# Kernel tuning notes

Hardware: AMD Instinct MI355X
Metric: run time of the kernel (lower is better)

The kernel has to match this reference:

```python
import jax, jax.numpy as jnp
import numpy as np

N_HEADS = 16
KQ_DIM = 64
EMB_DIM = 1024
CTX_DIM = 1024
EPS = 1e-5

def _layernorm(x, w, b):
    # LayerNorm over last dim (kq_dim), elementwise affine
    mu = jnp.mean(x, axis=-1, keepdims=True)
    var = jnp.mean(jnp.square(x - mu), axis=-1, keepdims=True)
    return (x - mu) * jax.lax.rsqrt(var + EPS) * w + b

def setup_inputs() -> dict:
    key = jax.random.key(0)
    ks = jax.random.split(key, 10)
    B, SQ, SK = 2, 2048, 2048
    inner = N_HEADS * KQ_DIM
    s_e = 1.0 / np.sqrt(EMB_DIM)
    s_c = 1.0 / np.sqrt(CTX_DIM)
    s_i = 1.0 / np.sqrt(inner)
    return {
        "emb": jax.random.normal(ks[0], (B, SQ, EMB_DIM), jnp.float32),
        "context": jax.random.normal(ks[1], (B, SK, CTX_DIM), jnp.float32),
        "Wq": jax.random.uniform(ks[2], (inner, EMB_DIM), jnp.float32, -s_e, s_e),
        "Wk": jax.random.uniform(ks[3], (inner, CTX_DIM), jnp.float32, -s_c, s_c),
        "Wv": jax.random.uniform(ks[4], (inner, CTX_DIM), jnp.float32, -s_c, s_c),
        "Wu": jax.random.uniform(ks[5], (EMB_DIM, inner), jnp.float32, -s_i, s_i),
        "bu": jax.random.uniform(ks[6], (EMB_DIM,), jnp.float32, -s_i, s_i),
        "qn_w": jnp.ones((KQ_DIM,), jnp.float32),
        "qn_b": jnp.zeros((KQ_DIM,), jnp.float32),
        "kn_w": jnp.ones((KQ_DIM,), jnp.float32),
        "kn_b": jnp.zeros((KQ_DIM,), jnp.float32),
    }

def reference(emb, context, Wq, Wk, Wv, Wu, bu, qn_w, qn_b, kn_w, kn_b):
    B, SQ, _ = emb.shape
    SK = context.shape[1]
    # projections (no bias), reshape to [B, H, S, D]
    q = (emb @ Wq.T).reshape(B, SQ, N_HEADS, KQ_DIM).transpose(0, 2, 1, 3)
    k = (context @ Wk.T).reshape(B, SK, N_HEADS, KQ_DIM).transpose(0, 2, 1, 3)
    v = (context @ Wv.T).reshape(B, SK, N_HEADS, KQ_DIM).transpose(0, 2, 1, 3)
    q = _layernorm(q, qn_w, qn_b)
    k = _layernorm(k, kn_w, kn_b)
    scale = 1.0 / jnp.sqrt(jnp.asarray(KQ_DIM, emb.dtype))
    attn = jnp.einsum('bhqd,bhkd->bhqk', q, k) * scale
    attn = jax.nn.softmax(attn, axis=-1)
    out = jnp.einsum('bhqk,bhkd->bhqd', attn, v)
    out = out.transpose(0, 2, 1, 3).reshape(B, SQ, N_HEADS * KQ_DIM)
    return out @ Wu.T + bu
```

## Files before the change

### kernel.cpp

```cpp
#include <hip/hip_runtime.h>


typedef __attribute__((ext_vector_type(8)))  short bf16x8;
typedef __attribute__((ext_vector_type(4)))  short bf16x4;
typedef __attribute__((ext_vector_type(4)))  float f32x4;
typedef __attribute__((ext_vector_type(16))) float f32x16;
typedef __attribute__((ext_vector_type(4)))  unsigned int u32x4;

#define SM_SCALE 0.18033688f

typedef __attribute__((address_space(1))) const void cg_void;
typedef __attribute__((address_space(3))) void lds_void_t;

__device__ __forceinline__ void gl_lds16(const void* g, void* l){
  __builtin_amdgcn_global_load_lds((cg_void*)g, (lds_void_t*)l, 16, 0, 0);
}

__device__ __forceinline__ short f2b(float f){
  unsigned int u;
  __builtin_memcpy(&u, &f, 4);
  u += 0x7fffu + ((u >> 16) & 1u);
  return (short)(u >> 16);
}

__device__ __forceinline__ unsigned int cvtpk(float a, float b){
  unsigned int r;
  asm("v_cvt_pk_bf16_f32 %0, %1, %2" : "=v"(r) : "v"(a), "v"(b));
  return r;
}

__global__ __launch_bounds__(256) void cvt6_kernel(
    const float* __restrict__ emb, const float* __restrict__ ctx,
    const float* __restrict__ Wq, const float* __restrict__ Wk,
    const float* __restrict__ Wv, const float* __restrict__ Wu,
    short* __restrict__ o_emb, short* __restrict__ o_ctx,
    short* __restrict__ o_wq, short* __restrict__ o_wk,
    short* __restrict__ o_wv, short* __restrict__ o_wu)
{
  const long M1 = 1024L * 1024L, M4 = 4L * M1;
  long e = ((long)blockIdx.x * 256 + threadIdx.x) * 4;
  if (e >= 12L * M1) return;
  const float* src; short* dst; long off;
  if      (e <     M4)      { src = emb; dst = o_emb; off = e;           }
  else if (e < 2 * M4)      { src = ctx; dst = o_ctx; off = e - M4;      }
  else if (e < 2 * M4 + M1) { src = Wq;  dst = o_wq;  off = e - 2 * M4;  }
  else if (e < 2 * M4 + 2*M1){src = Wk;  dst = o_wk;  off = e - 2*M4 - M1;}
  else if (e < 2 * M4 + 3*M1){src = Wv;  dst = o_wv;  off = e - 2*M4 - 2*M1;}
  else                      { src = Wu;  dst = o_wu;  off = e - 2*M4 - 3*M1;}
  f32x4 v = *(const f32x4*)(src + off);
  bf16x4 o;
  o[0] = f2b(v[0]); o[1] = f2b(v[1]); o[2] = f2b(v[2]); o[3] = f2b(v[3]);
  *(bf16x4*)(dst + off) = o;
}

__global__ __launch_bounds__(256, 3) void gemm_qkv_kernel(
    const short* __restrict__ embh, const short* __restrict__ ctxh,
    const short* __restrict__ Wqh, const short* __restrict__ Wkh,
    const short* __restrict__ Wvh,
    short* __restrict__ qo, short* __restrict__ ko, short* __restrict__ vto,
    const float* __restrict__ qw, const float* __restrict__ qb,
    const float* __restrict__ kw, const float* __restrict__ kb)
{
  const int K = 1024;
  __shared__ short As[128 * 64];
  __shared__ short Bs[128 * 64];
  const int tid  = threadIdx.x;
  const int wave = tid >> 6, lane = tid & 63;
  const int quad = lane >> 4, r16 = lane & 15;
  const int wm = (wave >> 1) * 64, wn = (wave & 1) * 64;

  const int task = blockIdx.y;
  int bn, bm, N;
  const short *A, *B;
  if (task == 2){
    bn = (blockIdx.x & 31) * 128; bm = (blockIdx.x >> 5) * 128; N = 4096;
    A = Wvh; B = ctxh;
  } else {
    bm = (blockIdx.x & 31) * 128; bn = (blockIdx.x >> 5) * 128; N = 1024;
    A = task ? ctxh : embh; B = task ? Wkh : Wqh;
  }

  f32x4 acc[4][4];
#pragma unroll
  for (int i = 0; i < 4; i++)
#pragma unroll
    for (int j = 0; j < 4; j++)
      acc[i][j] = (f32x4){0.f, 0.f, 0.f, 0.f};

  const int sr7 = (lane >> 3) & 7;
  const size_t arow = (size_t)(bm + wave * 8 + (lane >> 3)) * K
                      + (((lane & 7) ^ sr7) * 8);
  const size_t brow = (size_t)(bn + wave * 8 + (lane >> 3)) * K
                      + (((lane & 7) ^ sr7) * 8);
  const int sw = ((quad ^ (r16 & 7)) << 3);

  for (int k0 = 0; k0 < K; k0 += 64){
#pragma unroll
    for (int i = 0; i < 4; i++)
      gl_lds16(A + arow + (size_t)32 * i * K + k0, &As[wave * 512 + i * 2048]);
#pragma unroll
    for (int i = 0; i < 4; i++)
      gl_lds16(B + brow + (size_t)32 * i * K + k0, &Bs[wave * 512 + i * 2048]);
    __syncthreads();
#pragma unroll
    for (int kk = 0; kk < 2; kk++){
      const int off = sw ^ (kk << 5);
      bf16x8 af[4], bq[4];
#pragma unroll
      for (int i = 0; i < 4; i++)
        af[i] = *(const bf16x8*)(&As[(wm + i*16 + r16) * 64 + off]);
#pragma unroll
      for (int j = 0; j < 4; j++)
        bq[j] = *(const bf16x8*)(&Bs[(wn + j*16 + r16) * 64 + off]);
#pragma unroll
      for (int i = 0; i < 4; i++)
#pragma unroll
        for (int j = 0; j < 4; j++)
          acc[i][j] = __builtin_amdgcn_mfma_f32_16x16x32_bf16(af[i], bq[j], acc[i][j], 0, 0, 0);
    }
    __syncthreads();
  }

  if (task < 2){
    short* Ch = task ? ko : qo;
    const float* lw = task ? kw : qw;
    const float* lb = task ? kb : qb;
    const float post = task ? 1.0f : SM_SCALE;
    float wv[4], bv[4];
#pragma unroll
    for (int j = 0; j < 4; j++){
      wv[j] = lw[j*16 + r16] * post;
      bv[j] = lb[j*16 + r16] * post;
    }
#pragma unroll
    for (int i = 0; i < 4; i++){
#pragma unroll
      for (int t = 0; t < 4; t++){
        float a[4];
#pragma unroll
        for (int j = 0; j < 4; j++) a[j] = acc[i][j][t];
        float s = a[0] + a[1] + a[2] + a[3];
        s += __shfl_xor(s, 1); s += __shfl_xor(s, 2);
        s += __shfl_xor(s, 4); s += __shfl_xor(s, 8);
        const float mu = s * 0.015625f;
        float d[4], sq = 0.f;
#pragma unroll
        for (int j = 0; j < 4; j++){ d[j] = a[j] - mu; sq += d[j]*d[j]; }
        sq += __shfl_xor(sq, 1); sq += __shfl_xor(sq, 2);
        sq += __shfl_xor(sq, 4); sq += __shfl_xor(sq, 8);
        const float si = rsqrtf(sq * 0.015625f + 1e-5f);
        const size_t row = (size_t)(bm + wm + i*16 + quad*4 + t);
#pragma unroll
        for (int j = 0; j < 4; j++)
          Ch[row * 1024 + (bn + wn + j*16 + r16)] = f2b(d[j] * si * wv[j] + bv[j]);
      }
    }
  } else {
#pragma unroll
    for (int i = 0; i < 4; i++){
#pragma unroll
      for (int j = 0; j < 4; j++){
        const int p = (r16 & 3) | ((j & 1) << 2) | (((r16 >> 2) & 1) << 3)
                      | (((r16 >> 3) & 1) << 4);
        const int col = ((bn + wn + j*16 + r16) & ~31) | p;
#pragma unroll
        for (int t = 0; t < 4; t++){
          const size_t row = (size_t)(bm + wm + i*16 + quad*4 + t);
          vto[row * (size_t)N + col] = f2b(acc[i][j][t]);
        }
      }
    }
  }
}

__global__ __launch_bounds__(256, 4) void gemm_out_kernel(
    const short* __restrict__ A, const short* __restrict__ B,
    float* __restrict__ Cf, const float* __restrict__ bias)
{
  const int K = 1024, N = 1024;
  __shared__ short As[64 * 64];
  __shared__ short Bs[64 * 64];
  const int tid  = threadIdx.x;
  const int wave = tid >> 6, lane = tid & 63;
  const int quad = lane >> 4, r16 = lane & 15;
  const int wm = (wave >> 1) * 32, wn = (wave & 1) * 32;
  const int bm = blockIdx.x * 64, bn = blockIdx.y * 64;

  f32x4 acc[2][2];
#pragma unroll
  for (int i = 0; i < 2; i++)
#pragma unroll
    for (int j = 0; j < 2; j++)
      acc[i][j] = (f32x4){0.f, 0.f, 0.f, 0.f};

  const int sr7 = (lane >> 3) & 7;
  const size_t arow = (size_t)(bm + wave * 8 + (lane >> 3)) * K
                      + (((lane & 7) ^ sr7) * 8);
  const size_t brow = (size_t)(bn + wave * 8 + (lane >> 3)) * K
                      + (((lane & 7) ^ sr7) * 8);
  const int sw = ((quad ^ (r16 & 7)) << 3);

  for (int k0 = 0; k0 < K; k0 += 64){
#pragma unroll
    for (int i = 0; i < 2; i++){
      gl_lds16(A + arow + (size_t)32 * i * K + k0, &As[wave * 512 + i * 2048]);
      gl_lds16(B + brow + (size_t)32 * i * K + k0, &Bs[wave * 512 + i * 2048]);
    }
    __syncthreads();
#pragma unroll
    for (int kk = 0; kk < 2; kk++){
      const int off = sw ^ (kk << 5);
      bf16x8 af[2], bq[2];
#pragma unroll
      for (int i = 0; i < 2; i++)
        af[i] = *(const bf16x8*)(&As[(wm + i*16 + r16) * 64 + off]);
#pragma unroll
      for (int j = 0; j < 2; j++)
        bq[j] = *(const bf16x8*)(&Bs[(wn + j*16 + r16) * 64 + off]);
#pragma unroll
      for (int i = 0; i < 2; i++)
#pragma unroll
        for (int j = 0; j < 2; j++)
          acc[i][j] = __builtin_amdgcn_mfma_f32_16x16x32_bf16(af[i], bq[j], acc[i][j], 0, 0, 0);
    }
    __syncthreads();
  }

#pragma unroll
  for (int i = 0; i < 2; i++){
#pragma unroll
    for (int j = 0; j < 2; j++){
      const int col = bn + wn + j*16 + r16;
#pragma unroll
      for (int t = 0; t < 4; t++){
        const size_t row = (size_t)(bm + wm + i*16 + quad*4 + t);
        Cf[row * N + col] = acc[i][j][t] + bias[col];
      }
    }
  }
}

__global__ __launch_bounds__(256, 2) void flash2_kernel(
    const short* __restrict__ Q, const short* __restrict__ K,
    const short* __restrict__ Vt, short* __restrict__ O)
{
  __shared__ __align__(16) long long smem8[8192];
  short* Ks  = (short*)smem8;
  short* Vts = Ks + 16384;
  float* scr = (float*)smem8;

  const int tid = threadIdx.x;
  const int wave = tid >> 6, lane = tid & 63;
  const int half = wave >> 1, wg = wave & 1;
  const int hh = lane >> 5, q5 = lane & 31;
  const int h = blockIdx.x, qb = blockIdx.y, b = blockIdx.z;
  const int q0 = qb * 128 + wg * 64;

  const size_t kbase = ((size_t)b * 2048) * 1024 + (size_t)h * 64;
  const size_t vbase = ((size_t)h * 64) * 4096 + (size_t)b * 2048;

  bf16x8 qf[2][4];
#pragma unroll
  for (int qg = 0; qg < 2; qg++){
    const size_t qrow = ((size_t)b * 2048 + q0 + qg * 32 + q5) * 1024 + (size_t)h * 64;
#pragma unroll
    for (int c = 0; c < 4; c++)
      qf[qg][c] = *(const bf16x8*)(Q + qrow + c * 16 + hh * 8);
  }

  f32x16 oacc[2][2];
#pragma unroll
  for (int t = 0; t < 16; t++){
    oacc[0][0][t] = 0.f; oacc[0][1][t] = 0.f;
    oacc[1][0][t] = 0.f; oacc[1][1][t] = 0.f;
  }
  float lacc[2] = {0.f, 0.f};

  f32x16 zero16;
#pragma unroll
  for (int t = 0; t < 16; t++) zero16[t] = 0.f;

  const int srow = lane >> 3;
  const int csrc = ((lane & 7) ^ srow) * 8;
  const int wr0 = wg * 32;

#define STAGE(bufi, kt)                                                         \
  {                                                                             \
    const short* ks = K + kbase + (size_t)((kt) * 64 + wr0 + srow) * 1024 + csrc; \
    const short* vs = Vt + vbase + (size_t)(wr0 + srow) * 4096 + (kt) * 64 + csrc; \
    short* kd = Ks  + (half * 2 + (bufi)) * 4096 + wr0 * 64;                    \
    short* vd = Vts + (half * 2 + (bufi)) * 4096 + wr0 * 64;                    \
    gl_lds16(ks,             kd);                                               \
    gl_lds16(ks +  8 * 1024, kd + 512);                                         \
    gl_lds16(ks + 16 * 1024, kd + 1024);                                        \
    gl_lds16(ks + 24 * 1024, kd + 1536);                                        \
    gl_lds16(vs,             vd);                                               \
    gl_lds16(vs +  8 * 4096, vd + 512);                                         \
    gl_lds16(vs + 16 * 4096, vd + 1024);                                        \
    gl_lds16(vs + 24 * 4096, vd + 1536);                                        \
  }

  STAGE(0, half)

  for (int i = 0; i < 16; i++){
    const int buf = i & 1;
    __syncthreads();
    if (i + 1 < 16) STAGE(buf ^ 1, 2 * (i + 1) + half)

    const short* kb_l = Ks  + (half * 2 + buf) * 4096;
    const short* vb_l = Vts + (half * 2 + buf) * 4096;

    bf16x8 kf[2][4];
#pragma unroll
    for (int s32 = 0; s32 < 2; s32++){
      const int key = s32 * 32 + q5;
#pragma unroll
      for (int c = 0; c < 4; c++)
        kf[s32][c] = *(const bf16x8*)(&kb_l[key * 64 + (((2*c + hh) ^ (key & 7)) << 3)]);
    }

    f32x16 sacc[2][2];
    __builtin_amdgcn_s_setprio(1);
    sacc[0][0] = __builtin_amdgcn_mfma_f32_32x32x16_bf16(kf[0][0], qf[0][0], zero16, 0, 0, 0);
    sacc[0][1] = __builtin_amdgcn_mfma_f32_32x32x16_bf16(kf[1][0], qf[0][0], zero16, 0, 0, 0);
    sacc[1][0] = __builtin_amdgcn_mfma_f32_32x32x16_bf16(kf[0][0], qf[1][0], zero16, 0, 0, 0);
    sacc[1][1] = __builtin_amdgcn_mfma_f32_32x32x16_bf16(kf[1][0], qf[1][0], zero16, 0, 0, 0);
#pragma unroll
    for (int c = 1; c < 4; c++){
      sacc[0][0] = __builtin_amdgcn_mfma_f32_32x32x16_bf16(kf[0][c], qf[0][c], sacc[0][0], 0, 0, 0);
      sacc[0][1] = __builtin_amdgcn_mfma_f32_32x32x16_bf16(kf[1][c], qf[0][c], sacc[0][1], 0, 0, 0);
      sacc[1][0] = __builtin_amdgcn_mfma_f32_32x32x16_bf16(kf[0][c], qf[1][c], sacc[1][0], 0, 0, 0);
      sacc[1][1] = __builtin_amdgcn_mfma_f32_32x32x16_bf16(kf[1][c], qf[1][c], sacc[1][1], 0, 0, 0);
    }
    __builtin_amdgcn_s_setprio(0);

    bf16x8 pf[2][2][2];
#pragma unroll
    for (int qg = 0; qg < 2; qg++){
#pragma unroll
      for (int s32 = 0; s32 < 2; s32++){
        float e[16];
        float pp[4] = {0.f, 0.f, 0.f, 0.f};
#pragma unroll
        for (int t = 0; t < 16; t++){
          e[t] = __builtin_amdgcn_exp2f(sacc[qg][s32][t]);
          pp[t & 3] += e[t];
        }
        lacc[qg] += (pp[0] + pp[1]) + (pp[2] + pp[3]);
#pragma unroll
        for (int c = 0; c < 2; c++){
          u32x4 tmp;
          tmp[0] = cvtpk(e[4*c + 0],     e[4*c + 1]);
          tmp[1] = cvtpk(e[4*c + 2],     e[4*c + 3]);
          tmp[2] = cvtpk(e[8 + 4*c + 0], e[8 + 4*c + 1]);
          tmp[3] = cvtpk(e[8 + 4*c + 2], e[8 + 4*c + 3]);
          __builtin_memcpy(&pf[qg][s32][c], &tmp, 16);
        }
      }
    }

    __builtin_amdgcn_s_setprio(1);
#pragma unroll
    for (int s32 = 0; s32 < 2; s32++){
#pragma unroll
      for (int c = 0; c < 2; c++){
#pragma unroll
        for (int mt = 0; mt < 2; mt++){
          const int d = mt * 32 + q5;
          bf16x8 vf = *(const bf16x8*)(&vb_l[d * 64 + (((s32*4 + 2*c + hh) ^ (d & 7)) << 3)]);
          oacc[0][mt] = __builtin_amdgcn_mfma_f32_32x32x16_bf16(vf, pf[0][s32][c], oacc[0][mt], 0, 0, 0);
          oacc[1][mt] = __builtin_amdgcn_mfma_f32_32x32x16_bf16(vf, pf[1][s32][c], oacc[1][mt], 0, 0, 0);
        }
      }
    }
    __builtin_amdgcn_s_setprio(0);
  }

  const int widx = wg * 64 + lane;
  __syncthreads();
#pragma unroll
  for (int qg = 0; qg < 2; qg++){
    const float lh = lacc[qg] + __shfl_xor(lacc[qg], 32);
    if (half == 1){
      float* base = scr + widx * 33;
#pragma unroll
      for (int t = 0; t < 16; t++){ base[t] = oacc[qg][0][t]; base[16 + t] = oacc[qg][1][t]; }
      scr[4224 + widx] = lh;
    }
    __syncthreads();
    if (half == 0){
      const float* base = scr + widx * 33;
      const float l2 = scr[4224 + widx];
      const float linv = 1.0f / (lh + l2);
      const size_t orow = ((size_t)b * 2048 + q0 + qg * 32 + q5) * 1024 + (size_t)h * 64;
#pragma unroll
      for (int mt = 0; mt < 2; mt++){
#pragma unroll
        for (int g = 0; g < 4; g++){
          bf16x4 o4;
#pragma unroll
          for (int u = 0; u < 4; u++)
            o4[u] = f2b((oacc[qg][mt][g*4 + u] + base[mt*16 + g*4 + u]) * linv);
          *(bf16x4*)(O + orow + mt*32 + g*8 + 4*hh) = o4;
        }
      }
    }
    __syncthreads();
  }
}
#undef STAGE

extern "C" void kernel_launch(void* const* d_in, const int* in_sizes, int n_in,
                              void* d_out, int out_size, void* d_ws, size_t ws_size,
                              hipStream_t stream) {
  const float* emb  = (const float*)d_in[0];
  const float* ctx  = (const float*)d_in[1];
  const float* Wq   = (const float*)d_in[2];
  const float* Wk   = (const float*)d_in[3];
  const float* Wv   = (const float*)d_in[4];
  const float* Wu   = (const float*)d_in[5];
  const float* bu   = (const float*)d_in[6];
  const float* qn_w = (const float*)d_in[7];
  const float* qn_b = (const float*)d_in[8];
  const float* kn_w = (const float*)d_in[9];
  const float* kn_b = (const float*)d_in[10];
  float* out = (float*)d_out;

  const size_t BIG = (size_t)4096 * 1024;
  const size_t WSZ = (size_t)1024 * 1024;
  short* ws   = (short*)d_ws;
  short* embh = ws;
  short* ctxh = embh + BIG;
  short* Wqh  = ctxh + BIG;
  short* Wkh  = Wqh + WSZ;
  short* Wvh  = Wkh + WSZ;
  short* Wuh  = Wvh + WSZ;
  short* qh   = Wuh + WSZ;
  short* kh   = qh + BIG;
  short* vth  = kh + BIG;
  short* aoh  = vth + BIG;

  cvt6_kernel<<<12288, 256, 0, stream>>>(emb, ctx, Wq, Wk, Wv, Wu,
                                         embh, ctxh, Wqh, Wkh, Wvh, Wuh);

  gemm_qkv_kernel<<<dim3(256, 3), 256, 0, stream>>>(
      embh, ctxh, Wqh, Wkh, Wvh, qh, kh, vth,
      qn_w, qn_b, kn_w, kn_b);

  flash2_kernel<<<dim3(16, 16, 2), 256, 0, stream>>>(qh, kh, vth, aoh);

  gemm_out_kernel<<<dim3(64, 16), 256, 0, stream>>>(aoh, Wuh, out, bu);
}
```

Before: 197.5 us.

## Split flash attention keys across four wave pairs and enlarge output GEMM tile

The attention kernel now runs 512 threads per block, with four wave-pair groups each handling a 32-key slice per iteration instead of two groups on 64-key slices. It reduces the four partial outputs and row sums through LDS at the end, and drops the s_setprio hints. This aims to raise waves per CU and hide latency, at the cost of a larger cross-group reduction and smaller per-wave MFMA batches. The output GEMM also doubles its M tile to 128 rows per block, reusing each B tile more, while halving the grid and lowering the occupancy hint.

```diff
diff --git a/kernel.cpp b/kernel.cpp
--- a/kernel.cpp
+++ b/kernel.cpp
@@ -173,22 +173,22 @@
   }
 }
 
-__global__ __launch_bounds__(256, 4) void gemm_out_kernel(
+__global__ __launch_bounds__(256, 3) void gemm_out_kernel(
     const short* __restrict__ A, const short* __restrict__ B,
     float* __restrict__ Cf, const float* __restrict__ bias)
 {
   const int K = 1024, N = 1024;
-  __shared__ short As[64 * 64];
+  __shared__ short As[128 * 64];
   __shared__ short Bs[64 * 64];
   const int tid  = threadIdx.x;
   const int wave = tid >> 6, lane = tid & 63;
   const int quad = lane >> 4, r16 = lane & 15;
-  const int wm = (wave >> 1) * 32, wn = (wave & 1) * 32;
-  const int bm = blockIdx.x * 64, bn = blockIdx.y * 64;
-
-  f32x4 acc[2][2];
-#pragma unroll
-  for (int i = 0; i < 2; i++)
+  const int wm = (wave >> 1) * 64, wn = (wave & 1) * 32;
+  const int bm = blockIdx.x * 128, bn = blockIdx.y * 64;
+
+  f32x4 acc[4][2];
+#pragma unroll
+  for (int i = 0; i < 4; i++)
 #pragma unroll
     for (int j = 0; j < 2; j++)
       acc[i][j] = (f32x4){0.f, 0.f, 0.f, 0.f};
@@ -202,23 +202,24 @@
 
   for (int k0 = 0; k0 < K; k0 += 64){
 #pragma unroll
-    for (int i = 0; i < 2; i++){
+    for (int i = 0; i < 4; i++)
       gl_lds16(A + arow + (size_t)32 * i * K + k0, &As[wave * 512 + i * 2048]);
+#pragma unroll
+    for (int i = 0; i < 2; i++)
       gl_lds16(B + brow + (size_t)32 * i * K + k0, &Bs[wave * 512 + i * 2048]);
-    }
     __syncthreads();
 #pragma unroll
     for (int kk = 0; kk < 2; kk++){
       const int off = sw ^ (kk << 5);
-      bf16x8 af[2], bq[2];
-#pragma unroll
-      for (int i = 0; i < 2; i++)
+      bf16x8 af[4], bq[2];
+#pragma unroll
+      for (int i = 0; i < 4; i++)
         af[i] = *(const bf16x8*)(&As[(wm + i*16 + r16) * 64 + off]);
 #pragma unroll
       for (int j = 0; j < 2; j++)
         bq[j] = *(const bf16x8*)(&Bs[(wn + j*16 + r16) * 64 + off]);
 #pragma unroll
-      for (int i = 0; i < 2; i++)
+      for (int i = 0; i < 4; i++)
 #pragma unroll
         for (int j = 0; j < 2; j++)
           acc[i][j] = __builtin_amdgcn_mfma_f32_16x16x32_bf16(af[i], bq[j], acc[i][j], 0, 0, 0);
@@ -227,7 +228,7 @@
   }
 
 #pragma unroll
-  for (int i = 0; i < 2; i++){
+  for (int i = 0; i < 4; i++){
 #pragma unroll
     for (int j = 0; j < 2; j++){
       const int col = bn + wn + j*16 + r16;
@@ -240,7 +241,7 @@
   }
 }
 
-__global__ __launch_bounds__(256, 2) void flash2_kernel(
+__global__ __launch_bounds__(512, 4) void flash2_kernel(
     const short* __restrict__ Q, const short* __restrict__ K,
     const short* __restrict__ Vt, short* __restrict__ O)
 {
@@ -251,7 +252,7 @@
 
   const int tid = threadIdx.x;
   const int wave = tid >> 6, lane = tid & 63;
-  const int half = wave >> 1, wg = wave & 1;
+  const int ks4 = wave >> 1, wg = wave & 1;
   const int hh = lane >> 5, q5 = lane & 31;
   const int h = blockIdx.x, qb = blockIdx.y, b = blockIdx.z;
   const int q0 = qb * 128 + wg * 64;
@@ -280,100 +281,79 @@
 #pragma unroll
   for (int t = 0; t < 16; t++) zero16[t] = 0.f;
 
-  const int srow = lane >> 3;
-  const int csrc = ((lane & 7) ^ srow) * 8;
-  const int wr0 = wg * 32;
-
-#define STAGE(bufi, kt)                                                         \
-  {                                                                             \
-    const short* ks = K + kbase + (size_t)((kt) * 64 + wr0 + srow) * 1024 + csrc; \
-    const short* vs = Vt + vbase + (size_t)(wr0 + srow) * 4096 + (kt) * 64 + csrc; \
-    short* kd = Ks  + (half * 2 + (bufi)) * 4096 + wr0 * 64;                    \
-    short* vd = Vts + (half * 2 + (bufi)) * 4096 + wr0 * 64;                    \
-    gl_lds16(ks,             kd);                                               \
-    gl_lds16(ks +  8 * 1024, kd + 512);                                         \
-    gl_lds16(ks + 16 * 1024, kd + 1024);                                        \
-    gl_lds16(ks + 24 * 1024, kd + 1536);                                        \
-    gl_lds16(vs,             vd);                                               \
-    gl_lds16(vs +  8 * 4096, vd + 512);                                         \
-    gl_lds16(vs + 16 * 4096, vd + 1024);                                        \
-    gl_lds16(vs + 24 * 4096, vd + 1536);                                        \
-  }
-
-  STAGE(0, half)
+  const int srow  = lane >> 3;
+  const int kcsrc = ((lane & 7) ^ srow) * 8;
+  const int vrow  = lane >> 2;
+  const int vcsrc = ((lane & 3) ^ (vrow & 3)) * 8;
+
+#define STAGE(bufi, kt)                                                          \
+  {                                                                              \
+    const short* ks = K + kbase + (size_t)((kt) * 32 + wg * 16 + srow) * 1024 + kcsrc; \
+    const short* vs = Vt + vbase + (size_t)(wg * 32 + vrow) * 4096 + (kt) * 32 + vcsrc; \
+    short* kd = Ks  + (ks4 * 2 + (bufi)) * 2048 + wg * 1024;                     \
+    short* vd = Vts + (ks4 * 2 + (bufi)) * 2048 + wg * 1024;                     \
+    gl_lds16(ks,             kd);                                                \
+    gl_lds16(ks +  8 * 1024, kd + 512);                                          \
+    gl_lds16(vs,             vd);                                                \
+    gl_lds16(vs + 16 * 4096, vd + 512);                                          \
+  }
+
+  STAGE(0, ks4)
 
   for (int i = 0; i < 16; i++){
     const int buf = i & 1;
     __syncthreads();
-    if (i + 1 < 16) STAGE(buf ^ 1, 2 * (i + 1) + half)
-
-    const short* kb_l = Ks  + (half * 2 + buf) * 4096;
-    const short* vb_l = Vts + (half * 2 + buf) * 4096;
-
-    bf16x8 kf[2][4];
-#pragma unroll
-    for (int s32 = 0; s32 < 2; s32++){
-      const int key = s32 * 32 + q5;
-#pragma unroll
-      for (int c = 0; c < 4; c++)
-        kf[s32][c] = *(const bf16x8*)(&kb_l[key * 64 + (((2*c + hh) ^ (key & 7)) << 3)]);
-    }
-
-    f32x16 sacc[2][2];
-    __builtin_amdgcn_s_setprio(1);
-    sacc[0][0] = __builtin_amdgcn_mfma_f32_32x32x16_bf16(kf[0][0], qf[0][0], zero16, 0, 0, 0);
-    sacc[0][1] = __builtin_amdgcn_mfma_f32_32x32x16_bf16(kf[1][0], qf[0][0], zero16, 0, 0, 0);
-    sacc[1][0] = __builtin_amdgcn_mfma_f32_32x32x16_bf16(kf[0][0], qf[1][0], zero16, 0, 0, 0);
-    sacc[1][1] = __builtin_amdgcn_mfma_f32_32x32x16_bf16(kf[1][0], qf[1][0], zero16, 0, 0, 0);
+    if (i + 1 < 16) STAGE(buf ^ 1, 4 * (i + 1) + ks4)
+
+    const short* kb_l = Ks  + (ks4 * 2 + buf) * 2048;
+    const short* vb_l = Vts + (ks4 * 2 + buf) * 2048;
+
+    bf16x8 kf[4];
+#pragma unroll
+    for (int c = 0; c < 4; c++)
+      kf[c] = *(const bf16x8*)(&kb_l[q5 * 64 + (((2*c + hh) ^ (q5 & 7)) << 3)]);
+
+    f32x16 sacc[2];
+    sacc[0] = __builtin_amdgcn_mfma_f32_32x32x16_bf16(kf[0], qf[0][0], zero16, 0, 0, 0);
+    sacc[1] = __builtin_amdgcn_mfma_f32_32x32x16_bf16(kf[0], qf[1][0], zero16, 0, 0, 0);
 #pragma unroll
     for (int c = 1; c < 4; c++){
-      sacc[0][0] = __builtin_amdgcn_mfma_f32_32x32x16_bf16(kf[0][c], qf[0][c], sacc[0][0], 0, 0, 0);
-      sacc[0][1] = __builtin_amdgcn_mfma_f32_32x32x16_bf16(kf[1][c], qf[0][c], sacc[0][1], 0, 0, 0);
-      sacc[1][0] = __builtin_amdgcn_mfma_f32_32x32x16_bf16(kf[0][c], qf[1][c], sacc[1][0], 0, 0, 0);
-      sacc[1][1] = __builtin_amdgcn_mfma_f32_32x32x16_bf16(kf[1][c], qf[1][c], sacc[1][1], 0, 0, 0);
-    }
-    __builtin_amdgcn_s_setprio(0);
-
-    bf16x8 pf[2][2][2];
+      sacc[0] = __builtin_amdgcn_mfma_f32_32x32x16_bf16(kf[c], qf[0][c], sacc[0], 0, 0, 0);
+      sacc[1] = __builtin_amdgcn_mfma_f32_32x32x16_bf16(kf[c], qf[1][c], sacc[1], 0, 0, 0);
+    }
+
+    bf16x8 pf[2][2];
 #pragma unroll
     for (int qg = 0; qg < 2; qg++){
-#pragma unroll
-      for (int s32 = 0; s32 < 2; s32++){
-        float e[16];
-        float pp[4] = {0.f, 0.f, 0.f, 0.f};
-#pragma unroll
-        for (int t = 0; t < 16; t++){
-          e[t] = __builtin_amdgcn_exp2f(sacc[qg][s32][t]);
-          pp[t & 3] += e[t];
-        }
-        lacc[qg] += (pp[0] + pp[1]) + (pp[2] + pp[3]);
-#pragma unroll
-        for (int c = 0; c < 2; c++){
-          u32x4 tmp;
-          tmp[0] = cvtpk(e[4*c + 0],     e[4*c + 1]);
-          tmp[1] = cvtpk(e[4*c + 2],     e[4*c + 3]);
-          tmp[2] = cvtpk(e[8 + 4*c + 0], e[8 + 4*c + 1]);
-          tmp[3] = cvtpk(e[8 + 4*c + 2], e[8 + 4*c + 3]);
-          __builtin_memcpy(&pf[qg][s32][c], &tmp, 16);
-        }
-      }
-    }
-
-    __builtin_amdgcn_s_setprio(1);
-#pragma unroll
-    for (int s32 = 0; s32 < 2; s32++){
+      float e[16];
+      float pp[4] = {0.f, 0.f, 0.f, 0.f};
+#pragma unroll
+      for (int t = 0; t < 16; t++){
+        e[t] = __builtin_amdgcn_exp2f(sacc[qg][t]);
+        pp[t & 3] += e[t];
+      }
+      lacc[qg] += (pp[0] + pp[1]) + (pp[2] + pp[3]);
 #pragma unroll
       for (int c = 0; c < 2; c++){
-#pragma unroll
-        for (int mt = 0; mt < 2; mt++){
-          const int d = mt * 32 + q5;
-          bf16x8 vf = *(const bf16x8*)(&vb_l[d * 64 + (((s32*4 + 2*c + hh) ^ (d & 7)) << 3)]);
-          oacc[0][mt] = __builtin_amdgcn_mfma_f32_32x32x16_bf16(vf, pf[0][s32][c], oacc[0][mt], 0, 0, 0);
-          oacc[1][mt] = __builtin_amdgcn_mfma_f32_32x32x16_bf16(vf, pf[1][s32][c], oacc[1][mt], 0, 0, 0);
-        }
-      }
-    }
-    __builtin_amdgcn_s_setprio(0);
+        u32x4 tmp;
+        tmp[0] = cvtpk(e[4*c + 0],     e[4*c + 1]);
+        tmp[1] = cvtpk(e[4*c + 2],     e[4*c + 3]);
+        tmp[2] = cvtpk(e[8 + 4*c + 0], e[8 + 4*c + 1]);
+        tmp[3] = cvtpk(e[8 + 4*c + 2], e[8 + 4*c + 3]);
+        __builtin_memcpy(&pf[qg][c], &tmp, 16);
+      }
+    }
+
+#pragma unroll
+    for (int c = 0; c < 2; c++){
+#pragma unroll
+      for (int mt = 0; mt < 2; mt++){
+        const int d = mt * 32 + q5;
+        bf16x8 vf = *(const bf16x8*)(&vb_l[d * 32 + (((2*c + hh) ^ (d & 3)) << 3)]);
+        oacc[0][mt] = __builtin_amdgcn_mfma_f32_32x32x16_bf16(vf, pf[0][c], oacc[0][mt], 0, 0, 0);
+        oacc[1][mt] = __builtin_amdgcn_mfma_f32_32x32x16_bf16(vf, pf[1][c], oacc[1][mt], 0, 0, 0);
+      }
+    }
   }
 
   const int widx = wg * 64 + lane;
@@ -381,17 +361,26 @@
 #pragma unroll
   for (int qg = 0; qg < 2; qg++){
     const float lh = lacc[qg] + __shfl_xor(lacc[qg], 32);
-    if (half == 1){
-      float* base = scr + widx * 33;
+    if (ks4 != 0){
+      float* base = scr + ((ks4 - 1) * 128 + widx) * 33;
 #pragma unroll
       for (int t = 0; t < 16; t++){ base[t] = oacc[qg][0][t]; base[16 + t] = oacc[qg][1][t]; }
-      scr[4224 + widx] = lh;
-    }
-    __syncthreads();
-    if (half == 0){
-      const float* base = scr + widx * 33;
-      const float l2 = scr[4224 + widx];
-      const float linv = 1.0f / (lh + l2);
+      scr[12672 + (ks4 - 1) * 128 + widx] = lh;
+    }
+    __syncthreads();
+    if (ks4 == 0){
+      float ob[32];
+#pragma unroll
+      for (int t = 0; t < 16; t++){ ob[t] = oacc[qg][0][t]; ob[16 + t] = oacc[qg][1][t]; }
+      float lsum = lh;
+#pragma unroll
+      for (int w = 0; w < 3; w++){
+        const float* base = scr + (w * 128 + widx) * 33;
+#pragma unroll
+        for (int t = 0; t < 32; t++) ob[t] += base[t];
+        lsum += scr[12672 + w * 128 + widx];
+      }
+      const float linv = 1.0f / lsum;
       const size_t orow = ((size_t)b * 2048 + q0 + qg * 32 + q5) * 1024 + (size_t)h * 64;
 #pragma unroll
       for (int mt = 0; mt < 2; mt++){
@@ -400,7 +389,7 @@
           bf16x4 o4;
 #pragma unroll
           for (int u = 0; u < 4; u++)
-            o4[u] = f2b((oacc[qg][mt][g*4 + u] + base[mt*16 + g*4 + u]) * linv);
+            o4[u] = f2b(ob[mt*16 + g*4 + u] * linv);
           *(bf16x4*)(O + orow + mt*32 + g*8 + 4*hh) = o4;
         }
       }
@@ -447,7 +436,7 @@
       embh, ctxh, Wqh, Wkh, Wvh, qh, kh, vth,
       qn_w, qn_b, kn_w, kn_b);
 
-  flash2_kernel<<<dim3(16, 16, 2), 256, 0, stream>>>(qh, kh, vth, aoh);
-
-  gemm_out_kernel<<<dim3(64, 16), 256, 0, stream>>>(aoh, Wuh, out, bu);
-}
+  flash2_kernel<<<dim3(16, 16, 2), 512, 0, stream>>>(qh, kh, vth, aoh);
+
+  gemm_out_kernel<<<dim3(32, 16), 256, 0, stream>>>(aoh, Wuh, out, bu);
+}
```

New measurement: 254.0 us. +28.6%, slower.
